# Optimization experiments

Measured on AMD Instinct MI355X. Metric: run time of the kernel, lower is better.

The kernel has to match this reference:

```python
import jax, jax.numpy as jnp
import numpy as np

B, N, E, H, MAXLEN = 64, 256, 1024, 16, 512
D = E // H
LN_EPS = 1e-5
NORM_EPS = 1e-12


def setup_inputs() -> dict:
    key = jax.random.key(0)
    ks = jax.random.split(key, 12)
    s = 1.0 / np.sqrt(E)
    return {
        "news_embeds": jax.random.normal(ks[0], (B, N, E), jnp.float32),
        "padding_mask": jax.random.uniform(ks[1], (B, N)) > 0.8,  # True = padded
        "cls_token": jax.random.normal(ks[2], (1, 1, E), jnp.float32),
        "pos_emb": jax.random.normal(ks[3], (MAXLEN + 1, E), jnp.float32) * 0.02,
        "in_proj_w": jax.random.normal(ks[4], (3 * E, E), jnp.float32) * s,
        "in_proj_b": jnp.zeros((3 * E,), jnp.float32),
        "out_proj_w": jax.random.normal(ks[5], (E, E), jnp.float32) * s,
        "out_proj_b": jnp.zeros((E,), jnp.float32),
        "proj_w": jax.random.normal(ks[6], (E, E), jnp.float32) * s,
        "proj_b": jnp.zeros((E,), jnp.float32),
        "ln_gamma": jnp.ones((E,), jnp.float32),
        "ln_beta": jnp.zeros((E,), jnp.float32),
    }


def reference(news_embeds, padding_mask, cls_token, pos_emb, in_proj_w, in_proj_b,
              out_proj_w, out_proj_b, proj_w, proj_b, ln_gamma, ln_beta):
    b, n, e = news_embeds.shape
    S = n + 1
    # prepend CLS token, add positional encodings (dropout inactive in eval)
    x = jnp.concatenate([jnp.broadcast_to(cls_token, (b, 1, e)), news_embeds], axis=1)
    x = x + pos_emb[:S][None, :, :]
    # key padding mask with CLS always attendable
    mask = jnp.concatenate(
        [jnp.zeros((b, 1), dtype=bool), padding_mask], axis=1)  # [b,S]
    # packed QKV projection (nn.MultiheadAttention in_proj)
    qkv = jnp.einsum('bse,fe->bsf', x, in_proj_w) + in_proj_b
    q, k, v = jnp.split(qkv, 3, axis=-1)
    q = q.reshape(b, S, H, D)
    k = k.reshape(b, S, H, D)
    v = v.reshape(b, S, H, D)
    scores = jnp.einsum('bqhd,bkhd->bhqk', q, k) / jnp.sqrt(
        jnp.asarray(D, x.dtype))
    big_neg = jnp.asarray(-1e9, scores.dtype)
    scores = jnp.where(mask[:, None, None, :], big_neg, scores)
    attn = jax.nn.softmax(scores, axis=-1)  # [b,H,S,S]
    ctx = jnp.einsum('bhqk,bkhd->bqhd', attn, v).reshape(b, S, e)
    attn_out = jnp.einsum('bse,fe->bsf', ctx, out_proj_w) + out_proj_b
    # projection head: Linear -> (Dropout eval noop) -> LayerNorm -> ReLU
    p = jnp.einsum('bse,fe->bsf', attn_out, proj_w) + proj_b
    mu = jnp.mean(p, axis=-1, keepdims=True)
    var = jnp.var(p, axis=-1, keepdims=True)
    ln = (p - mu) * jax.lax.rsqrt(var + LN_EPS) * ln_gamma + ln_beta
    proj = jax.nn.relu(ln)
    user = proj[:, 0, :]
    norm = jnp.maximum(jnp.linalg.norm(user, axis=-1, keepdims=True), NORM_EPS)
    user = user / norm
    return user, attn
```

## Files before the change

### kernel.cpp

```cpp
#include <hip/hip_runtime.h>

#define B_   64
#define N_   256
#define E_   1024
#define H_   16
#define D_   64
#define S_   257
#define M_   16448
#define MP2  16640
#define N3_  3072
#define K_   1024

typedef unsigned short u16;
typedef unsigned int   u32;
typedef __bf16 bf16x8 __attribute__((ext_vector_type(8)));
typedef float  f32x4  __attribute__((ext_vector_type(4)));

__device__ inline u16 f2bf(float f) {
  union { float f; u32 u; } a; a.f = f;
  return (u16)((a.u + 0x7FFFu + ((a.u >> 16) & 1u)) >> 16);
}
__device__ inline float bf2f(u16 h) {
  union { u32 u; float f; } a; a.u = ((u32)h) << 16; return a.f;
}
__device__ inline void gload_lds16(const void* g, void* l) {
  __builtin_amdgcn_global_load_lds((const __attribute__((address_space(1))) void*)g,
                                   (__attribute__((address_space(3))) void*)l, 16, 0, 0);
}

__global__ __launch_bounds__(256) void prep_w(const float* __restrict__ w, u16* __restrict__ o) {
  size_t i = ((size_t)blockIdx.x * 256 + threadIdx.x) * 4;
  float4 f = *(const float4*)(w + i);
  ushort4 v;
  v.x = f2bf(f.x); v.y = f2bf(f.y); v.z = f2bf(f.z); v.w = f2bf(f.w);
  *(ushort4*)(o + i) = v;
}

__global__ __launch_bounds__(256) void build_x(const float* __restrict__ news,
                                               const float* __restrict__ cls,
                                               const float* __restrict__ pos,
                                               u16* __restrict__ x) {
  const int row = blockIdx.x;
  const int e = threadIdx.x * 4;
  float4 v = make_float4(0.f, 0.f, 0.f, 0.f);
  if (row < M_) {
    const int b = row / S_;
    const int s = row - b * S_;
    float4 pe = *(const float4*)(pos + (size_t)s * E_ + e);
    float4 xv = (s == 0) ? *(const float4*)(cls + e)
                         : *(const float4*)(news + ((size_t)b * N_ + (s - 1)) * E_ + e);
    v.x = xv.x + pe.x; v.y = xv.y + pe.y; v.z = xv.z + pe.z; v.w = xv.w + pe.w;
  }
  ushort4 o;
  o.x = f2bf(v.x); o.y = f2bf(v.y); o.z = f2bf(v.z); o.w = f2bf(v.w);
  *(ushort4*)(x + (size_t)row * E_ + e) = o;
}

__global__ __launch_bounds__(256) void mask_prep(const void* __restrict__ src, int* __restrict__ dst) {
  const int t = threadIdx.x;
  const u32* wsrc = (const u32*)src;
  u32 flag = 0;
  for (int i = t; i < 4096; i += 256) {
    u32 v = wsrc[i];
    if (v == 0x3F800000u) flag |= 2u;
    else if (v > 1u) flag |= 1u;
  }
  __shared__ u32 fsh;
  if (t == 0) fsh = 0;
  __syncthreads();
  if (flag) atomicOr(&fsh, flag);
  __syncthreads();
  const u32 f = fsh;
  const int mode = (f & 2u) ? 2 : ((f & 1u) ? 1 : 0);
  const int base = blockIdx.x * 2048;
  for (int i = base + t; i < base + 2048; i += 256) {
    int m;
    if (mode == 0)      m = (wsrc[i] != 0u);
    else if (mode == 2) m = (((const float*)src)[i] != 0.f);
    else                m = (((const unsigned char*)src)[i] != 0);
    dst[i] = m;
  }
}

__global__ __launch_bounds__(256) void gemm_qkv(const u16* __restrict__ A,
                                                const u16* __restrict__ Bw,
                                                const float* __restrict__ bias,
                                                u16* __restrict__ C) {
  __shared__ u16 As[128 * 32];
  __shared__ u16 Bs[128 * 32];
  const int t = threadIdx.x;
  const int w = t >> 6, l = t & 63;
  const int wr = w >> 1, wc = w & 1;

  const int orig = blockIdx.x;
  const int wgid = (orig & 7) * 390 + (orig >> 3);
  const int bm = wgid / 24, bn = wgid % 24;

  const u16* Ab = A + (size_t)bm * 128 * K_;
  const u16* Bb = Bw + (size_t)bn * 128 * K_;
  f32x4 acc[4][4] = {};
  const int r0 = t >> 2,         col0 = (t & 3) << 3;
  const int r1 = (256 + t) >> 2, col1 = ((256 + t) & 3) << 3;
  char* AsB = (char*)As + w * 1024;
  char* BsB = (char*)Bs + w * 1024;

  for (int k0 = 0; k0 < K_; k0 += 32) {
    gload_lds16(Ab + (size_t)r0 * K_ + k0 + col0, AsB);
    gload_lds16(Ab + (size_t)r1 * K_ + k0 + col1, AsB + 4096);
    gload_lds16(Bb + (size_t)r0 * K_ + k0 + col0, BsB);
    gload_lds16(Bb + (size_t)r1 * K_ + k0 + col1, BsB + 4096);
    __syncthreads();
    const int kc = (l >> 4) << 3;
    bf16x8 af[4], bfr[4];
#pragma unroll
    for (int m = 0; m < 4; ++m)
      af[m] = *(const bf16x8*)&As[(wr * 64 + m * 16 + (l & 15)) * 32 + kc];
#pragma unroll
    for (int n = 0; n < 4; ++n)
      bfr[n] = *(const bf16x8*)&Bs[(wc * 64 + n * 16 + (l & 15)) * 32 + kc];
#pragma unroll
    for (int m = 0; m < 4; ++m)
#pragma unroll
      for (int n = 0; n < 4; ++n)
        acc[m][n] = __builtin_amdgcn_mfma_f32_16x16x32_bf16(af[m], bfr[n], acc[m][n], 0, 0, 0);
    __syncthreads();
  }
  const int row0 = bm * 128 + wr * 64 + ((l >> 4) << 2);
  const int colb = bn * 128 + wc * 64 + (l & 15);
#pragma unroll
  for (int n = 0; n < 4; ++n) {
    const int col = colb + n * 16;
    const float bv = bias[col];
#pragma unroll
    for (int m = 0; m < 4; ++m) {
      const int row = row0 + m * 16;
#pragma unroll
      for (int j = 0; j < 4; ++j)
        C[(size_t)(row + j) * N3_ + col] = f2bf(acc[m][n][j] + bv);
    }
  }
}

__global__ __launch_bounds__(256) void attn_kernel(const u16* __restrict__ qkv,
                                                   const int* __restrict__ maskw,
                                                   float* __restrict__ attn,
                                                   float* __restrict__ ctx) {
  __shared__ u16 Ks[258 * 72];
  __shared__ float msk[272];
  __shared__ float p0[272];
  __shared__ float red[4][64];
  const int qt = blockIdx.x, h = blockIdx.y, b = blockIdx.z;
  const int t = threadIdx.x;
  const int q0 = qt * 64;

  for (int c = t; c < 258 * 8; c += 256) {
    const int r = c >> 3, qq = c & 7;
    uint4 val = make_uint4(0, 0, 0, 0);
    if (r < S_)
      val = *(const uint4*)(qkv + (size_t)(b * S_ + r) * N3_ + E_ + h * 64 + qq * 8);
    *(uint4*)&Ks[r * 72 + qq * 8] = val;
  }
  for (int i = t; i < 272; i += 256) {
    float m = 0.f;
    if (i == 0) m = 1.f;
    else if (i < S_) m = maskw[b * N_ + i - 1] ? 0.f : 1.f;
    msk[i] = m;
  }
  __syncthreads();

  const int w = t >> 6, l = t & 63;
  const int cl = l & 15, rg = l >> 4;
  const int kc = rg * 8;

  const u16* qrow = qkv + (size_t)(b * S_ + q0 + w * 16 + cl) * N3_ + h * 64 + kc;
  const bf16x8 qa0 = *(const bf16x8*)qrow;
  const bf16x8 qa1 = *(const bf16x8*)(qrow + 32);

  u32 pk[17][2];
  float sum[4] = {0.f, 0.f, 0.f, 0.f};
#pragma unroll
  for (int kt = 0; kt < 17; ++kt) {
    int krow = kt * 16 + cl;
    if (krow > 257) krow = 257;
    const u16* kb = &Ks[krow * 72 + kc];
    f32x4 a = {0.f, 0.f, 0.f, 0.f};
    a = __builtin_amdgcn_mfma_f32_16x16x32_bf16(qa0, *(const bf16x8*)kb, a, 0, 0, 0);
    a = __builtin_amdgcn_mfma_f32_16x16x32_bf16(qa1, *(const bf16x8*)(kb + 32), a, 0, 0, 0);
    const float m = msk[kt * 16 + cl];
    u16 h0[4];
#pragma unroll
    for (int j = 0; j < 4; ++j) {
      h0[j] = f2bf(m * __expf(a[j] * 0.125f));
      sum[j] += bf2f(h0[j]);
    }
    pk[kt][0] = (u32)h0[0] | ((u32)h0[1] << 16);
    pk[kt][1] = (u32)h0[2] | ((u32)h0[3] << 16);
  }
  float inv[4];
#pragma unroll
  for (int j = 0; j < 4; ++j) {
#pragma unroll
    for (int o = 1; o < 16; o <<= 1) sum[j] += __shfl_xor(sum[j], o);
    inv[j] = 1.f / sum[j];
  }

  const int qrow0 = q0 + w * 16 + rg * 4;
  float* abase = attn + (size_t)(b * H_ + h) * S_ * S_;
  const bool isCls = (qt == 0 && w == 0 && rg == 0);
#pragma unroll
  for (int j = 0; j < 4; ++j) {
    const int gq = qrow0 + j;
    if (gq < S_) {
      float* arow = abase + (size_t)gq * S_;
#pragma unroll
      for (int kt = 0; kt < 17; ++kt) {
        const int col = kt * 16 + cl;
        if (col < S_) {
          const u16 hh = (u16)(pk[kt][j >> 1] >> ((j & 1) * 16));
          arow[col] = bf2f(hh) * inv[j];
        }
      }
    }
  }
  if (isCls) {
#pragma unroll
    for (int kt = 0; kt < 17; ++kt) {
      const u16 hh = (u16)(pk[kt][0] & 0xFFFFu);
      p0[kt * 16 + cl] = bf2f(hh) * inv[0];
    }
  }

  if (qt == 0) {
    __syncthreads();
    const int part = t >> 6, d = t & 63;
    float acc = 0.f;
    for (int k = part; k < S_; k += 4)
      acc = fmaf(p0[k], bf2f(qkv[(size_t)(b * S_ + k) * N3_ + 2 * E_ + h * 64 + d]), acc);
    red[part][d] = acc;
    __syncthreads();
    if (t < 64)
      ctx[(size_t)b * E_ + h * 64 + t] = red[0][t] + red[1][t] + red[2][t] + red[3][t];
  }
}

__global__ __launch_bounds__(256) void gemv_cls(const float* __restrict__ in,
                                                const float* __restrict__ W,
                                                const float* __restrict__ bias,
                                                float* __restrict__ out) {
  const int bt = blockIdx.x, fc = blockIdx.y, t = threadIdx.x;
  __shared__ float xs[4][E_];
  for (int i = t; i < E_; i += 256)
    ((float4*)xs)[i] = ((const float4*)(in + (size_t)bt * 4 * E_))[i];
  __syncthreads();
  const int f = fc * 64 + (t >> 2);
  const int ec = (t & 3) * 256;
  const float4* wr = (const float4*)(W + (size_t)f * E_ + ec);
  float a0 = 0.f, a1 = 0.f, a2 = 0.f, a3 = 0.f;
#pragma unroll 8
  for (int e4 = 0; e4 < 64; ++e4) {
    const float4 wv = wr[e4];
    const float4 x0 = *(const float4*)&xs[0][ec + e4 * 4];
    const float4 x1 = *(const float4*)&xs[1][ec + e4 * 4];
    const float4 x2 = *(const float4*)&xs[2][ec + e4 * 4];
    const float4 x3 = *(const float4*)&xs[3][ec + e4 * 4];
    a0 += wv.x * x0.x + wv.y * x0.y + wv.z * x0.z + wv.w * x0.w;
    a1 += wv.x * x1.x + wv.y * x1.y + wv.z * x1.z + wv.w * x1.w;
    a2 += wv.x * x2.x + wv.y * x2.y + wv.z * x2.z + wv.w * x2.w;
    a3 += wv.x * x3.x + wv.y * x3.y + wv.z * x3.z + wv.w * x3.w;
  }
  a0 += __shfl_xor(a0, 1); a0 += __shfl_xor(a0, 2);
  a1 += __shfl_xor(a1, 1); a1 += __shfl_xor(a1, 2);
  a2 += __shfl_xor(a2, 1); a2 += __shfl_xor(a2, 2);
  a3 += __shfl_xor(a3, 1); a3 += __shfl_xor(a3, 2);
  if ((t & 3) == 0) {
    const float bv = bias[f];
    out[(size_t)(bt * 4 + 0) * E_ + f] = a0 + bv;
    out[(size_t)(bt * 4 + 1) * E_ + f] = a1 + bv;
    out[(size_t)(bt * 4 + 2) * E_ + f] = a2 + bv;
    out[(size_t)(bt * 4 + 3) * E_ + f] = a3 + bv;
  }
}

__global__ __launch_bounds__(256) void ln_relu_norm(const float* __restrict__ p,
                                                    const float* __restrict__ gamma,
                                                    const float* __restrict__ beta,
                                                    float* __restrict__ user) {
  const int b = blockIdx.x, t = threadIdx.x;
  const int w = t >> 6, l = t & 63;
  const float4 v = ((const float4*)(p + (size_t)b * E_))[t];
  float s = v.x + v.y + v.z + v.w;
  float s2 = v.x * v.x + v.y * v.y + v.z * v.z + v.w * v.w;
#pragma unroll
  for (int o = 1; o < 64; o <<= 1) { s += __shfl_xor(s, o); s2 += __shfl_xor(s2, o); }
  __shared__ float ss[4], ss2[4], qs[4];
  if (l == 0) { ss[w] = s; ss2[w] = s2; }
  __syncthreads();
  s = ss[0] + ss[1] + ss[2] + ss[3];
  s2 = ss2[0] + ss2[1] + ss2[2] + ss2[3];
  const float mu = s * (1.f / E_);
  const float var = s2 * (1.f / E_) - mu * mu;
  const float rstd = rsqrtf(var + 1e-5f);
  const float4 g = ((const float4*)gamma)[t];
  const float4 be = ((const float4*)beta)[t];
  float4 o;
  o.x = fmaxf((v.x - mu) * rstd * g.x + be.x, 0.f);
  o.y = fmaxf((v.y - mu) * rstd * g.y + be.y, 0.f);
  o.z = fmaxf((v.z - mu) * rstd * g.z + be.z, 0.f);
  o.w = fmaxf((v.w - mu) * rstd * g.w + be.w, 0.f);
  float q2 = o.x * o.x + o.y * o.y + o.z * o.z + o.w * o.w;
#pragma unroll
  for (int off = 1; off < 64; off <<= 1) q2 += __shfl_xor(q2, off);
  if (l == 0) qs[w] = q2;
  __syncthreads();
  q2 = qs[0] + qs[1] + qs[2] + qs[3];
  const float nrm = fmaxf(sqrtf(q2), 1e-12f);
  const float inv = 1.f / nrm;
  float4 u;
  u.x = o.x * inv; u.y = o.y * inv; u.z = o.z * inv; u.w = o.w * inv;
  ((float4*)(user + (size_t)b * E_))[t] = u;
}

extern "C" void kernel_launch(void* const* d_in, const int* in_sizes, int n_in,
                              void* d_out, int out_size, void* d_ws, size_t ws_size,
                              hipStream_t stream) {
  const float* news   = (const float*)d_in[0];
  const void*  maskp  = d_in[1];
  const float* cls    = (const float*)d_in[2];
  const float* pos    = (const float*)d_in[3];
  const float* w_in   = (const float*)d_in[4];
  const float* b_in   = (const float*)d_in[5];
  const float* w_out  = (const float*)d_in[6];
  const float* b_out  = (const float*)d_in[7];
  const float* w_proj = (const float*)d_in[8];
  const float* b_proj = (const float*)d_in[9];
  const float* gamma  = (const float*)d_in[10];
  const float* beta   = (const float*)d_in[11];

  char* ws = (char*)d_ws;
  u16*  w_bf  = (u16*)(ws + 0);
  u16*  x_bf  = (u16*)(ws + 6291456);
  u16*  qkv   = (u16*)(ws + 40370176);
  float* ctx  = (float*)(ws + 142606336);
  float* aoc  = (float*)(ws + 142868480);
  float* pcls = (float*)(ws + 143130624);
  int*  maskw = (int*)(ws + 143392768);

  float* user = (float*)d_out;
  float* attn = (float*)d_out + (size_t)B_ * E_;

  prep_w<<<3072, 256, 0, stream>>>(w_in, w_bf);
  build_x<<<MP2, 256, 0, stream>>>(news, cls, pos, x_bf);
  mask_prep<<<8, 256, 0, stream>>>(maskp, maskw);
  gemm_qkv<<<3120, 256, 0, stream>>>(x_bf, w_bf, b_in, qkv);
  attn_kernel<<<dim3(5, H_, B_), 256, 0, stream>>>(qkv, maskw, attn, ctx);
  gemv_cls<<<dim3(16, 16), 256, 0, stream>>>(ctx, w_out, b_out, aoc);
  gemv_cls<<<dim3(16, 16), 256, 0, stream>>>(aoc, w_proj, b_proj, pcls);
  ln_relu_norm<<<B_, 256, 0, stream>>>(pcls, gamma, beta, user);
}
```

Measured before the change: 347.4 us.

## Load K tile in two halves to shrink attention kernel shared memory

The attention kernel now stages K in two phases: rows 0-143 first, then the remaining rows into the same buffer after a barrier. This cuts the K shared-memory buffer from 258 to 144 rows, presumably to fit more blocks per CU. In exchange it adds two extra __syncthreads and serializes the second K load behind the first half of the score computation. The later part of the kernel must not reuse Ks for V-related work; it is unclear whether the hidden code depends on the full K buffer.

```diff
diff --git a/kernel.cpp b/kernel.cpp
--- a/kernel.cpp
+++ b/kernel.cpp
@@ -145,7 +145,7 @@
                                                    const int* __restrict__ maskw,
                                                    float* __restrict__ attn,
                                                    float* __restrict__ ctx) {
-  __shared__ u16 Ks[258 * 72];
+  __shared__ u16 Ks[144 * 72];
   __shared__ float msk[272];
   __shared__ float p0[272];
   __shared__ float red[4][64];
@@ -153,12 +153,10 @@
   const int t = threadIdx.x;
   const int q0 = qt * 64;
 
-  for (int c = t; c < 258 * 8; c += 256) {
+  for (int c = t; c < 144 * 8; c += 256) {
     const int r = c >> 3, qq = c & 7;
-    uint4 val = make_uint4(0, 0, 0, 0);
-    if (r < S_)
-      val = *(const uint4*)(qkv + (size_t)(b * S_ + r) * N3_ + E_ + h * 64 + qq * 8);
-    *(uint4*)&Ks[r * 72 + qq * 8] = val;
+    *(uint4*)&Ks[r * 72 + qq * 8] =
+        *(const uint4*)(qkv + (size_t)(b * S_ + r) * N3_ + E_ + h * 64 + qq * 8);
   }
   for (int i = t; i < 272; i += 256) {
     float m = 0.f;
@@ -178,11 +176,10 @@
 
   u32 pk[17][2];
   float sum[4] = {0.f, 0.f, 0.f, 0.f};
-#pragma unroll
-  for (int kt = 0; kt < 17; ++kt) {
-    int krow = kt * 16 + cl;
-    if (krow > 257) krow = 257;
-    const u16* kb = &Ks[krow * 72 + kc];
+
+#pragma unroll
+  for (int kt = 0; kt < 9; ++kt) {
+    const u16* kb = &Ks[(kt * 16 + cl) * 72 + kc];
     f32x4 a = {0.f, 0.f, 0.f, 0.f};
     a = __builtin_amdgcn_mfma_f32_16x16x32_bf16(qa0, *(const bf16x8*)kb, a, 0, 0, 0);
     a = __builtin_amdgcn_mfma_f32_16x16x32_bf16(qa1, *(const bf16x8*)(kb + 32), a, 0, 0, 0);
@@ -196,6 +193,37 @@
     pk[kt][0] = (u32)h0[0] | ((u32)h0[1] << 16);
     pk[kt][1] = (u32)h0[2] | ((u32)h0[3] << 16);
   }
+  __syncthreads();
+
+  for (int c = t; c < 114 * 8; c += 256) {
+    const int r = c >> 3, qq = c & 7;
+    const int g = 144 + r;
+    uint4 val = make_uint4(0, 0, 0, 0);
+    if (g < S_)
+      val = *(const uint4*)(qkv + (size_t)(b * S_ + g) * N3_ + E_ + h * 64 + qq * 8);
+    *(uint4*)&Ks[r * 72 + qq * 8] = val;
+  }
+  __syncthreads();
+
+#pragma unroll
+  for (int kt = 9; kt < 17; ++kt) {
+    int krow = kt * 16 + cl;
+    if (krow > 257) krow = 257;
+    const u16* kb = &Ks[(krow - 144) * 72 + kc];
+    f32x4 a = {0.f, 0.f, 0.f, 0.f};
+    a = __builtin_amdgcn_mfma_f32_16x16x32_bf16(qa0, *(const bf16x8*)kb, a, 0, 0, 0);
+    a = __builtin_amdgcn_mfma_f32_16x16x32_bf16(qa1, *(const bf16x8*)(kb + 32), a, 0, 0, 0);
+    const float m = msk[kt * 16 + cl];
+    u16 h0[4];
+#pragma unroll
+    for (int j = 0; j < 4; ++j) {
+      h0[j] = f2bf(m * __expf(a[j] * 0.125f));
+      sum[j] += bf2f(h0[j]);
+    }
+    pk[kt][0] = (u32)h0[0] | ((u32)h0[1] << 16);
+    pk[kt][1] = (u32)h0[2] | ((u32)h0[3] << 16);
+  }
+
   float inv[4];
 #pragma unroll
   for (int j = 0; j < 4; ++j) {
```

Result: no change. 345.5 us, median of 2 (-0.6%).
